# Performance work log

Hardware: AMD Instinct MI355X
Metric: run time of the kernel (lower is better)

## Reference

```python
import jax, jax.numpy as jnp
import numpy as np

# ---- static configuration (from init_kwargs) ----
L = 36.0            # cubic cell edge (bohr)
G = 180             # grid points per axis
NA = 64             # number of atoms
NRAD = 8            # basis['n']
NL = 4              # basis['l']
RO = 2.5            # basis['r_o'] (bohr)
A = L / G           # grid spacing (orthorhombic -> U = diag(A))
RMAX = int(np.ceil(RO / A))          # half-width of periodic box (13)
B = 2 * RMAX + 1                     # box edge (27)
VCELL = A ** 3                       # |det U|
# static coefficient mask: keep (n,l,m) with |m - NL| <= l  (same as tril*flip(tril))
_MASK = np.abs(np.arange(2 * NL + 1)[None, :] - NL) <= np.arange(NL)[:, None]


def _make_W():
    # orthonormalization matrix W = S^{-1/2} for radials phi_n(r) = r^2 (r_o - r)^{n+2}
    r = np.linspace(0.0, RO, 4000)
    phi = np.stack([r ** 2 * (RO - r) ** (n + 2) for n in range(NRAD)])
    S = np.trapz(phi[:, None] * phi[None, :], r, axis=-1)
    w, v = np.linalg.eigh(S)
    return (v @ np.diag(w ** -0.5) @ v.T).astype(np.float32)


def setup_inputs() -> dict:
    key = jax.random.key(0)
    k1, k2 = jax.random.split(key)
    rho = jax.random.uniform(k1, (G, G, G), dtype=jnp.float32)       # electron density >= 0
    positions = jax.random.uniform(k2, (NA, 3), dtype=jnp.float32) * L
    return {"rho": rho, "positions": positions, "W": jnp.asarray(_make_W())}


def _sph_padded(theta, phi):
    # real spherical harmonics, zero-padded to [NL, 2*NL+1, ...] with m at index NL+m
    ct = jnp.cos(theta); st = jnp.sin(theta)
    cp = jnp.cos(phi); sp = jnp.sin(phi)
    c2p = jnp.cos(2 * phi); s2p = jnp.sin(2 * phi)
    c3p = jnp.cos(3 * phi); s3p = jnp.sin(3 * phi)
    z = jnp.zeros_like(theta)
    one = jnp.ones_like(theta)
    Y = {
        (0, 0): 0.28209479177387814 * one,
        (1, -1): 0.4886025119029199 * st * sp,
        (1, 0): 0.4886025119029199 * ct,
        (1, 1): 0.4886025119029199 * st * cp,
        (2, -2): 0.5462742152960396 * st ** 2 * s2p,
        (2, -1): 1.0925484305920792 * st * ct * sp,
        (2, 0): 0.31539156525252005 * (3 * ct ** 2 - 1),
        (2, 1): 1.0925484305920792 * st * ct * cp,
        (2, 2): 0.5462742152960396 * st ** 2 * c2p,
        (3, -3): 0.5900435899266435 * st ** 3 * s3p,
        (3, -2): 1.445305721320277 * st ** 2 * ct * s2p,
        (3, -1): 0.4570457994644658 * st * (5 * ct ** 2 - 1) * sp,
        (3, 0): 0.3731763325901154 * (5 * ct ** 3 - 3 * ct),
        (3, 1): 0.4570457994644658 * st * (5 * ct ** 2 - 1) * cp,
        (3, 2): 1.445305721320277 * st ** 2 * ct * c2p,
        (3, 3): 0.5900435899266435 * st ** 3 * c3p,
    }
    rows = []
    for l in range(NL):
        pad = [z] * (NL - l)
        rows.append(jnp.stack(pad + [Y[(l, m)] for m in range(-l, l + 1)] + pad))
    return jnp.stack(rows)  # [NL, 2NL+1, B, B, B]


def _project_atom(rho, pos, W):
    a = jnp.float32(A)
    cm = jnp.round(pos / a)            # nearest grid index of atom (U_inv @ pos)
    dr = pos - a * cm                  # sub-grid displacement
    offs = jnp.arange(-RMAX, RMAX + 1, dtype=jnp.float32)
    # periodic mesh indices (box_around / fmod wrap)
    Xm = jnp.mod(offs + cm[0], G).astype(jnp.int32)
    Ym = jnp.mod(offs + cm[1], G).astype(jnp.int32)
    Zm = jnp.mod(offs + cm[2], G).astype(jnp.int32)
    srho = rho[Xm[:, None, None], Ym[None, :, None], Zm[None, None, :]]  # [B,B,B] gather
    # euclidean coords relative to the atom
    Xs = (offs * a - dr[0])[:, None, None]
    Ys = (offs * a - dr[1])[None, :, None]
    Zs = (offs * a - dr[2])[None, None, :]
    Xs, Ys, Zs = jnp.broadcast_arrays(Xs, Ys, Zs)
    R = jnp.sqrt(Xs ** 2 + Ys ** 2 + Zs ** 2)
    Rsafe = jnp.where(R < 1e-12, 1.0, R)
    Theta = jnp.where(R < 1e-12, 0.0, jnp.arccos(jnp.clip(Zs / Rsafe, -1.0, 1.0)))
    Phi = jnp.arctan2(Ys, Xs)
    angs = _sph_padded(Theta, Phi)                       # [NL, 2NL+1, B,B,B]
    ns = jnp.arange(NRAD, dtype=jnp.float32)[:, None, None, None]
    phi_n = jnp.where(R < RO, R ** 2 * jnp.maximum(RO - R, 0.0) ** (ns + 2.0), 0.0)
    rads = jnp.einsum('nm,mijk->nijk', W, phi_n) * jnp.float32(VCELL)  # [NRAD, B,B,B]
    coeff = jnp.einsum('lmijk,nijk,ijk->nlm', angs, rads, srho)        # [NRAD, NL, 2NL+1]
    return coeff[:, _MASK].reshape(-1)                    # [NRAD * NL^2] = 128


def reference(rho, positions, W):
    # vmap over atoms (single species -> identical box shape per atom)
    return jax.vmap(lambda p: _project_atom(rho, p, W))(positions)  # [NA, 128]
```

## Files before the change

kernel.cpp:

```cpp
#include <hip/hip_runtime.h>

#define G 180
#define NRAD 8
#define RO_F 2.5f
#define A_F 0.2f
#define VCELL_F 0.008f
#define CELLS 19683
#define SLABS 8
#define NATOMS 64


__global__ __launch_bounds__(256, 2) void proj_kernel(
    const float* __restrict__ rho, const float* __restrict__ pos,
    float* __restrict__ ws)
{
    const int atom = blockIdx.y;
    const int slab = blockIdx.x;
    const int tid  = threadIdx.x;
    const int lane = tid & 63;
    const int waveid = tid >> 6;

    const float px = pos[atom*3+0], py = pos[atom*3+1], pz = pos[atom*3+2];
    const float cmx = rintf(px * 5.0f), cmy = rintf(py * 5.0f), cmz = rintf(pz * 5.0f);
    const float drx = px - A_F*cmx, dry = py - A_F*cmy, drz = pz - A_F*cmz;
    const int icx = (int)cmx - 13, icy = (int)cmy - 13, icz = (int)cmz - 13;

    float acc[128];
    #pragma unroll
    for (int j = 0; j < 128; ++j) acc[j] = 0.0f;

    for (int c = slab*256 + tid; c < CELLS; c += SLABS*256) {
        int i = c / 729;
        int rem = c - i*729;
        int j = rem / 27;
        int k = rem - j*27;
        int gx = i + icx; gx += (gx < 0) ? G : 0; gx -= (gx >= G) ? G : 0;
        int gy = j + icy; gy += (gy < 0) ? G : 0; gy -= (gy >= G) ? G : 0;
        int gz = k + icz; gz += (gz < 0) ? G : 0; gz -= (gz >= G) ? G : 0;
        float s = rho[(gx*G + gy)*G + gz];

        float x = (float)(i-13)*A_F - drx;
        float y = (float)(j-13)*A_F - dry;
        float z = (float)(k-13)*A_F - drz;
        float r2 = x*x + y*y + z*z;
        float inv = rsqrtf(fmaxf(r2, 1e-24f));
        float R = r2 * inv;
        if (R < RO_F) {
            float t = RO_F - R;
            float ux = x*inv, uy = y*inv, uz = z*inv;
            float uz2 = uz*uz;
            float ux2 = ux*ux, uy2 = uy*uy;
            float ys[16];
            ys[0]  = 0.28209479177f * s;
            ys[1]  = 0.48860251190f * uy * s;
            ys[2]  = 0.48860251190f * uz * s;
            ys[3]  = 0.48860251190f * ux * s;
            ys[4]  = 1.09254843059f * ux*uy * s;
            ys[5]  = 1.09254843059f * uy*uz * s;
            ys[6]  = 0.31539156525f * (3.0f*uz2 - 1.0f) * s;
            ys[7]  = 1.09254843059f * ux*uz * s;
            ys[8]  = 0.54627421530f * (ux2 - uy2) * s;
            ys[9]  = 0.59004358993f * uy*(3.0f*ux2 - uy2) * s;
            ys[10] = 2.89061144264f * ux*uy*uz * s;
            ys[11] = 0.45704579946f * uy*(5.0f*uz2 - 1.0f) * s;
            ys[12] = 0.37317633259f * uz*(5.0f*uz2 - 3.0f) * s;
            ys[13] = 0.45704579946f * ux*(5.0f*uz2 - 1.0f) * s;
            ys[14] = 1.44530572132f * (ux2 - uy2)*uz * s;
            ys[15] = 0.59004358993f * ux*(ux2 - 3.0f*uy2) * s;

            float p = r2 * t * t;
            #pragma unroll
            for (int n = 0; n < NRAD; ++n) {
                #pragma unroll
                for (int q = 0; q < 16; ++q)
                    acc[n*16+q] = fmaf(p, ys[q], acc[n*16+q]);
                p *= t;
            }
        }
    }

    __shared__ float red[4][64][33];
    const int col  = lane & 31;
    const int half = lane >> 5;
    #pragma unroll
    for (int cb = 0; cb < 4; ++cb) {
        __syncthreads();
        #pragma unroll
        for (int q = 0; q < 32; ++q)
            red[waveid][lane][q] = acc[cb*32 + q];
        __syncthreads();
        float csum = 0.0f;
        #pragma unroll
        for (int r = 0; r < 32; ++r)
            csum += red[waveid][half*32 + r][col];
        atomicAdd(&ws[atom*128 + cb*32 + col], csum);
    }
}

__global__ void finalize_kernel(const float* __restrict__ ws,
                                const float* __restrict__ W,
                                float* __restrict__ out)
{
    const int atom = blockIdx.x;
    const int t = threadIdx.x;
    const int n = t >> 4, q = t & 15;
    float sum = 0.0f;
    #pragma unroll
    for (int k = 0; k < 8; ++k)
        sum = fmaf(W[n*8+k], ws[atom*128 + k*16 + q], sum);
    out[atom*128 + t] = sum * VCELL_F;
}

extern "C" void kernel_launch(void* const* d_in, const int* in_sizes, int n_in,
                              void* d_out, int out_size, void* d_ws, size_t ws_size,
                              hipStream_t stream) {
    const float* rho = (const float*)d_in[0];
    const float* pos = (const float*)d_in[1];
    const float* W   = (const float*)d_in[2];
    float* out = (float*)d_out;
    float* ws  = (float*)d_ws;

    hipMemsetAsync(ws, 0, NATOMS*128*sizeof(float), stream);
    dim3 grid(SLABS, NATOMS);
    proj_kernel<<<grid, 256, 0, stream>>>(rho, pos, ws);
    finalize_kernel<<<NATOMS, 128, 0, stream>>>(ws, W, out);
}
```

Measured before the change: 84.78 us.

## Split radial orders across waves and replace atomics with per-slab partial sums

Each of the four waves in a block now handles two radial orders (32 accumulators) over the slab's cells instead of every thread holding all 128 accumulators. This cuts register pressure so occupancy can rise, with launch bounds raised to 4 blocks per SM. The price is that each wave recomputes the cell geometry, the density load and the spherical harmonics for the same cells. The atomic adds and the memset are replaced by per-slab, per-wave partial-sum writes, which finalize_kernel now sums before applying W.

```diff
diff --git a/kernel.cpp b/kernel.cpp
--- a/kernel.cpp
+++ b/kernel.cpp
@@ -10,7 +10,8 @@
 #define NATOMS 64
 
 
-__global__ __launch_bounds__(256, 2) void proj_kernel(
+
+__global__ __launch_bounds__(256, 4) void proj_kernel(
     const float* __restrict__ rho, const float* __restrict__ pos,
     float* __restrict__ ws)
 {
@@ -18,18 +19,18 @@
     const int slab = blockIdx.x;
     const int tid  = threadIdx.x;
     const int lane = tid & 63;
-    const int waveid = tid >> 6;
+    const int w    = tid >> 6;
 
     const float px = pos[atom*3+0], py = pos[atom*3+1], pz = pos[atom*3+2];
     const float cmx = rintf(px * 5.0f), cmy = rintf(py * 5.0f), cmz = rintf(pz * 5.0f);
     const float drx = px - A_F*cmx, dry = py - A_F*cmy, drz = pz - A_F*cmz;
     const int icx = (int)cmx - 13, icy = (int)cmy - 13, icz = (int)cmz - 13;
 
-    float acc[128];
+    float acc[32];
     #pragma unroll
-    for (int j = 0; j < 128; ++j) acc[j] = 0.0f;
+    for (int j = 0; j < 32; ++j) acc[j] = 0.0f;
 
-    for (int c = slab*256 + tid; c < CELLS; c += SLABS*256) {
+    for (int c = slab*64 + lane; c < CELLS; c += SLABS*64) {
         int i = c / 729;
         int rem = c - i*729;
         int j = rem / 27;
@@ -51,49 +52,54 @@
             float uz2 = uz*uz;
             float ux2 = ux*ux, uy2 = uy*uy;
             float ys[16];
-            ys[0]  = 0.28209479177f * s;
-            ys[1]  = 0.48860251190f * uy * s;
-            ys[2]  = 0.48860251190f * uz * s;
-            ys[3]  = 0.48860251190f * ux * s;
-            ys[4]  = 1.09254843059f * ux*uy * s;
-            ys[5]  = 1.09254843059f * uy*uz * s;
-            ys[6]  = 0.31539156525f * (3.0f*uz2 - 1.0f) * s;
-            ys[7]  = 1.09254843059f * ux*uz * s;
-            ys[8]  = 0.54627421530f * (ux2 - uy2) * s;
-            ys[9]  = 0.59004358993f * uy*(3.0f*ux2 - uy2) * s;
-            ys[10] = 2.89061144264f * ux*uy*uz * s;
-            ys[11] = 0.45704579946f * uy*(5.0f*uz2 - 1.0f) * s;
-            ys[12] = 0.37317633259f * uz*(5.0f*uz2 - 3.0f) * s;
-            ys[13] = 0.45704579946f * ux*(5.0f*uz2 - 1.0f) * s;
-            ys[14] = 1.44530572132f * (ux2 - uy2)*uz * s;
-            ys[15] = 0.59004358993f * ux*(ux2 - 3.0f*uy2) * s;
+            ys[0]  = 0.28209479177f;
+            ys[1]  = 0.48860251190f * uy;
+            ys[2]  = 0.48860251190f * uz;
+            ys[3]  = 0.48860251190f * ux;
+            ys[4]  = 1.09254843059f * ux*uy;
+            ys[5]  = 1.09254843059f * uy*uz;
+            ys[6]  = 0.31539156525f * (3.0f*uz2 - 1.0f);
+            ys[7]  = 1.09254843059f * ux*uz;
+            ys[8]  = 0.54627421530f * (ux2 - uy2);
+            ys[9]  = 0.59004358993f * uy*(3.0f*ux2 - uy2);
+            ys[10] = 2.89061144264f * ux*uy*uz;
+            ys[11] = 0.45704579946f * uy*(5.0f*uz2 - 1.0f);
+            ys[12] = 0.37317633259f * uz*(5.0f*uz2 - 3.0f);
+            ys[13] = 0.45704579946f * ux*(5.0f*uz2 - 1.0f);
+            ys[14] = 1.44530572132f * (ux2 - uy2)*uz;
+            ys[15] = 0.59004358993f * ux*(ux2 - 3.0f*uy2);
 
-            float p = r2 * t * t;
+            float t2 = t*t;
+            float p = s * r2 * t2;
+            if (w >= 1) p *= t2;
+            if (w >= 2) p *= t2;
+            if (w >= 3) p *= t2;
+            float pt = p * t;
             #pragma unroll
-            for (int n = 0; n < NRAD; ++n) {
-                #pragma unroll
-                for (int q = 0; q < 16; ++q)
-                    acc[n*16+q] = fmaf(p, ys[q], acc[n*16+q]);
-                p *= t;
+            for (int q = 0; q < 16; ++q) {
+                acc[q]    = fmaf(p,  ys[q], acc[q]);
+                acc[16+q] = fmaf(pt, ys[q], acc[16+q]);
             }
         }
     }
 
     __shared__ float red[4][64][33];
+    __shared__ float stage[4][2][32];
+    #pragma unroll
+    for (int q = 0; q < 32; ++q)
+        red[w][lane][q] = acc[q];
+    __syncthreads();
     const int col  = lane & 31;
     const int half = lane >> 5;
+    float csum = 0.0f;
     #pragma unroll
-    for (int cb = 0; cb < 4; ++cb) {
-        __syncthreads();
-        #pragma unroll
-        for (int q = 0; q < 32; ++q)
-            red[waveid][lane][q] = acc[cb*32 + q];
-        __syncthreads();
-        float csum = 0.0f;
-        #pragma unroll
-        for (int r = 0; r < 32; ++r)
-            csum += red[waveid][half*32 + r][col];
-        atomicAdd(&ws[atom*128 + cb*32 + col], csum);
+    for (int r = 0; r < 32; ++r)
+        csum += red[w][half*32 + r][col];
+    stage[w][half][col] = csum;
+    __syncthreads();
+    if (lane < 32) {
+        float v = stage[w][0][lane] + stage[w][1][lane];
+        ws[((atom*SLABS + slab)*4 + w)*32 + lane] = v;
     }
 }
 
@@ -104,10 +110,21 @@
     const int atom = blockIdx.x;
     const int t = threadIdx.x;
     const int n = t >> 4, q = t & 15;
+    const float* base = ws + atom*SLABS*4*32;
+    float M[8];
+    #pragma unroll
+    for (int k = 0; k < 8; ++k) {
+        const int g = k >> 1, row = k & 1;
+        float sk = 0.0f;
+        #pragma unroll
+        for (int s = 0; s < 8; ++s)
+            sk += base[(s*4 + g)*32 + row*16 + q];
+        M[k] = sk;
+    }
     float sum = 0.0f;
     #pragma unroll
     for (int k = 0; k < 8; ++k)
-        sum = fmaf(W[n*8+k], ws[atom*128 + k*16 + q], sum);
+        sum = fmaf(W[n*8+k], M[k], sum);
     out[atom*128 + t] = sum * VCELL_F;
 }
 
@@ -120,7 +137,6 @@
     float* out = (float*)d_out;
     float* ws  = (float*)d_ws;
 
-    hipMemsetAsync(ws, 0, NATOMS*128*sizeof(float), stream);
     dim3 grid(SLABS, NATOMS);
     proj_kernel<<<grid, 256, 0, stream>>>(rho, pos, ws);
     finalize_kernel<<<NATOMS, 128, 0, stream>>>(ws, W, out);
```

Result: slower. 88.85 us (+4.8%).
